# Kernel optimization log

Hardware: AMD Instinct MI355X
Metric: run time of the kernel (lower is better)

## Reference

```python
import jax, jax.numpy as jnp
import numpy as np

B, S, INPUT_DIM = 8, 512, 64
D_MODEL, NUM_LAYERS, OUTPUT_DIM = 512, 4, 10
D_INNER, D_STATE, D_CONV, DT_RANK = 2 * D_MODEL, 16, 4, 32
GRID_SIZE, SPLINE_K = 5, 3
N_COEFF = GRID_SIZE + SPLINE_K  # 8
_H = 2.0 / GRID_SIZE
GRID = jnp.linspace(-1.0 - SPLINE_K * _H, 1.0 + SPLINE_K * _H, GRID_SIZE + 2 * SPLINE_K + 1)


def b_splines(x):
    # x: (..., in) -> (..., in, N_COEFF) via Cox-de Boor recursion on fixed GRID
    x = x[..., None]
    b = ((x >= GRID[:-1]) & (x < GRID[1:])).astype(x.dtype)
    for p in range(1, SPLINE_K + 1):
        left = (x - GRID[:-(p + 1)]) / (GRID[p:-1] - GRID[:-(p + 1)])
        right = (GRID[p + 1:] - x) / (GRID[p + 1:] - GRID[1:-p])
        b = left * b[..., :-1] + right * b[..., 1:]
    return b


def kan(x, base_w, spline_w):
    # efficient-KAN: silu base path + per-edge spline path
    return jax.nn.silu(x) @ base_w.T + jnp.einsum('...ik,oik->...o', b_splines(x), spline_w)


def layernorm(x, g, b):
    m = jnp.mean(x, -1, keepdims=True)
    v = jnp.var(x, -1, keepdims=True)
    return (x - m) / jnp.sqrt(v + 1e-5) * g + b


def liquid_proj(x, Win, Wrec, b, tau):
    # liquid time-constant RNN: h' = (tanh(Wx + Uh + b) - h) / tau
    pre = x @ Win  # (B,S,H)
    tau_pos = jax.nn.softplus(tau) + 0.1
    def step(h, p):
        act = jnp.tanh(p + h @ Wrec + b)
        h = h + (act - h) / tau_pos
        return h, h
    h0 = jnp.zeros((x.shape[0], Win.shape[1]), x.dtype)
    hT, hs = jax.lax.scan(step, h0, pre.transpose(1, 0, 2))
    return hs.transpose(1, 0, 2), hT


def mamba_block(x, in_proj_w, conv_w, conv_b, x_proj_w, dt_proj_w, dt_proj_b, A_log, Dp, out_proj_w):
    Bb, Ss, _ = x.shape
    xz = x @ in_proj_w.T                       # (B,S,2*di)
    xm, z = jnp.split(xz, 2, axis=-1)
    # causal depthwise conv1d with kernel D_CONV
    xp = jnp.pad(xm, ((0, 0), (D_CONV - 1, 0), (0, 0)))
    xm = sum(xp[:, k:k + Ss, :] * conv_w[:, k] for k in range(D_CONV)) + conv_b
    xm = jax.nn.silu(xm)
    x_dbl = xm @ x_proj_w.T                    # (B,S,dt_rank+2n)
    dt, Bc, Cc = jnp.split(x_dbl, [DT_RANK, DT_RANK + D_STATE], axis=-1)
    dt = jax.nn.softplus(dt @ dt_proj_w.T + dt_proj_b)   # (B,S,di)
    A = -jnp.exp(A_log)                        # (di,n)
    dA = jnp.exp(dt[..., None] * A)            # (B,S,di,n)
    dBu = dt[..., None] * Bc[:, :, None, :] * xm[..., None]
    def step(h, inp):
        a, bu, c = inp
        h = a * h + bu
        return h, jnp.einsum('bdn,bn->bd', h, c)
    h0 = jnp.zeros((Bb, D_INNER, D_STATE), x.dtype)
    _, ys = jax.lax.scan(step, h0, (dA.transpose(1, 0, 2, 3), dBu.transpose(1, 0, 2, 3), Cc.transpose(1, 0, 2)))
    y = ys.transpose(1, 0, 2) + Dp * xm
    y = y * jax.nn.silu(z)
    return y @ out_proj_w.T


def forward(x, lq_Win, lq_Wrec, lq_b, lq_tau, ln_g, ln_b, in_proj_w, conv_w, conv_b,
            x_proj_w, dt_proj_w, dt_proj_b, A_log, Dp, out_proj_w,
            kan_base_w, kan_spline_w, fn_g, fn_b, cls_base_w, cls_spline_w):
    x, _ = liquid_proj(x, lq_Win, lq_Wrec, lq_b, lq_tau)
    for l in range(NUM_LAYERS):
        residual = x
        xn = layernorm(x, ln_g[l], ln_b[l])
        xm = mamba_block(xn, in_proj_w[l], conv_w[l], conv_b[l], x_proj_w[l],
                         dt_proj_w[l], dt_proj_b[l], A_log[l], Dp[l], out_proj_w[l])
        x = residual + kan(xm, kan_base_w[l], kan_spline_w[l])
    x = layernorm(x, fn_g, fn_b)
    return kan(x.mean(axis=1), cls_base_w, cls_spline_w)


def setup_inputs():
    key = jax.random.key(0)
    ks = jax.random.split(key, 12)
    n = lambda k, shape, s: jax.random.normal(k, shape, jnp.float32) * s
    return {
        "x": n(ks[0], (B, S, INPUT_DIM), 1.0),
        "lq_Win": n(ks[1], (INPUT_DIM, D_MODEL), INPUT_DIM ** -0.5),
        "lq_Wrec": n(ks[2], (D_MODEL, D_MODEL), D_MODEL ** -0.5),
        "lq_b": jnp.zeros((D_MODEL,), jnp.float32),
        "lq_tau": jnp.ones((D_MODEL,), jnp.float32),
        "ln_g": jnp.ones((NUM_LAYERS, D_MODEL), jnp.float32),
        "ln_b": jnp.zeros((NUM_LAYERS, D_MODEL), jnp.float32),
        "in_proj_w": n(ks[3], (NUM_LAYERS, 2 * D_INNER, D_MODEL), D_MODEL ** -0.5),
        "conv_w": n(ks[4], (NUM_LAYERS, D_INNER, D_CONV), D_CONV ** -0.5),
        "conv_b": jnp.zeros((NUM_LAYERS, D_INNER), jnp.float32),
        "x_proj_w": n(ks[5], (NUM_LAYERS, DT_RANK + 2 * D_STATE, D_INNER), D_INNER ** -0.5),
        "dt_proj_w": n(ks[6], (NUM_LAYERS, D_INNER, DT_RANK), DT_RANK ** -0.5),
        "dt_proj_b": jnp.full((NUM_LAYERS, D_INNER), float(np.log(np.expm1(0.01))), jnp.float32),
        "A_log": jnp.log(jnp.broadcast_to(jnp.arange(1, D_STATE + 1, dtype=jnp.float32), (NUM_LAYERS, D_INNER, D_STATE))),
        "Dp": jnp.ones((NUM_LAYERS, D_INNER), jnp.float32),
        "out_proj_w": n(ks[7], (NUM_LAYERS, D_MODEL, D_INNER), D_INNER ** -0.5),
        "kan_base_w": n(ks[8], (NUM_LAYERS, D_MODEL, D_MODEL), D_MODEL ** -0.5),
        "kan_spline_w": n(ks[9], (NUM_LAYERS, D_MODEL, D_MODEL, N_COEFF), 0.1 * D_MODEL ** -0.5),
        "fn_g": jnp.ones((D_MODEL,), jnp.float32),
        "fn_b": jnp.zeros((D_MODEL,), jnp.float32),
        "cls_base_w": n(ks[10], (OUTPUT_DIM, D_MODEL), D_MODEL ** -0.5),
        "cls_spline_w": n(ks[11], (OUTPUT_DIM, D_MODEL, N_COEFF), 0.1 * D_MODEL ** -0.5),
    }


def reference(x, lq_Win, lq_Wrec, lq_b, lq_tau, ln_g, ln_b, in_proj_w, conv_w, conv_b,
              x_proj_w, dt_proj_w, dt_proj_b, A_log, Dp, out_proj_w,
              kan_base_w, kan_spline_w, fn_g, fn_b, cls_base_w, cls_spline_w):
    return forward(x, lq_Win, lq_Wrec, lq_b, lq_tau, ln_g, ln_b, in_proj_w, conv_w, conv_b,
                   x_proj_w, dt_proj_w, dt_proj_b, A_log, Dp, out_proj_w,
                   kan_base_w, kan_spline_w, fn_g, fn_b, cls_base_w, cls_spline_w)
```

## Files before the change

kernel.cpp:

```cpp
#include <hip/hip_runtime.h>
#include <hip/hip_bf16.h>
#include <cmath>

#define DEV __device__ __forceinline__

constexpr int B_ = 8, S_ = 512, IN_ = 64, D_ = 512, L_ = 4;
constexpr int DI_ = 1024, DCONV_ = 4, DTR_ = 32;
constexpr int ROWS = B_ * S_;

constexpr size_t MB = 1ull << 20;
constexpr size_t OFF_X    = 0;
constexpr size_t OFF_XN   = OFF_X   + 8*MB;
constexpr size_t OFF_XZ   = OFF_XN  + 8*MB;
constexpr size_t OFF_XM   = OFF_XZ  + 32*MB;
constexpr size_t OFF_DT   = OFF_XM  + 16*MB;
constexpr size_t OFF_XDBL = OFF_DT  + 16*MB;
constexpr size_t OFF_YG   = OFF_XDBL+ 1*MB;
constexpr size_t OFF_MO   = OFF_YG  + 16*MB;
constexpr size_t OFF_WINT = OFF_MO  + 8*MB;
constexpr size_t OFF_MEAN = OFF_WINT+ 128*1024;
constexpr size_t OFF_HBUF = OFF_MEAN+ 16*1024;
constexpr size_t OFF_FLG  = OFF_HBUF+ 32*1024;
constexpr size_t OFF_W16  = OFF_FLG + 64*1024;
constexpr size_t OFF_BASIS= OFF_XZ;

constexpr size_t W_IP = 0;
constexpr size_t W_OP = 1048576;
constexpr size_t W_KB = 1572864;
constexpr size_t W_KS = 1835008;
constexpr size_t W_XP = 3932160;
constexpr size_t W_DT = 3997696;
constexpr size_t W_PER_LAYER = 4030464;

DEV float siluf(float x){ return x / (1.f + __expf(-x)); }
DEV float softplusf(float x){ return fmaxf(x, 0.f) + log1pf(__expf(-fabsf(x))); }
DEV unsigned short f2h(float f){ return __builtin_bit_cast(unsigned short, (_Float16)f); }
DEV int pk2(float a, float b){ return (int)((unsigned)f2h(a) | ((unsigned)f2h(b) << 16)); }

typedef _Float16 half8 __attribute__((ext_vector_type(8)));
typedef float f32x4 __attribute__((ext_vector_type(4)));

DEV void bspline8(float x, float* bb){
  const float h = 0.4f, g0 = -2.2f;
  float b0[11];
#pragma unroll
  for (int j = 0; j < 11; ++j){
    float gj  = g0 + h * j;
    float gj1 = g0 + h * (j + 1);
    b0[j] = (x >= gj && x < gj1) ? 1.f : 0.f;
  }
#pragma unroll
  for (int p = 1; p <= 3; ++p){
    float inv = 1.f / (h * p);
#pragma unroll
    for (int j = 0; j + p < 11; ++j){
      float gj  = g0 + h * j;
      float gip = g0 + h * (j + p + 1);
      b0[j] = (x - gj) * inv * b0[j] + (gip - x) * inv * b0[j + 1];
    }
  }
#pragma unroll
  for (int c = 0; c < 8; ++c) bb[c] = b0[c];
}

__global__ __launch_bounds__(256)
void conv_w16(const float* __restrict__ ip, const float* __restrict__ op,
              const float* __restrict__ kb, const float* __restrict__ ks,
              const float* __restrict__ xp, const float* __restrict__ dt,
              unsigned short* __restrict__ w16)
{
  int blk = blockIdx.x, tid = threadIdx.x;
  const float* src; size_t doff; int sb;
  if      (blk < 512) { src = ip; doff = W_IP; sb = blk; }
  else if (blk < 768) { src = op; doff = W_OP; sb = blk - 512; }
  else if (blk < 896) { src = kb; doff = W_KB; sb = blk - 768; }
  else if (blk < 1920){ src = ks; doff = W_KS; sb = blk - 896; }
  else if (blk < 1952){ src = xp; doff = W_XP; sb = blk - 1920; }
  else                { src = dt; doff = W_DT; sb = blk - 1952; }
  size_t e = (size_t)sb * 2048 + tid * 8;
  float4 a = *(const float4*)(src + e), b = *(const float4*)(src + e + 4);
  int4 v = { pk2(a.x,a.y), pk2(a.z,a.w), pk2(b.x,b.y), pk2(b.z,b.w) };
  *(int4*)&w16[doff + e] = v;
}

template<bool SILU_A, int EPI>
__global__ __launch_bounds__(256)
void gemm_nt(const float* __restrict__ A, int lda,
             const float* __restrict__ W, int ldw,
             float* __restrict__ C, int ldc,
             const float* __restrict__ bias, int K)
{
  __shared__ float As[16][68];
  __shared__ float Ws[16][68];
  const int tid = threadIdx.x;
  const int m0 = blockIdx.y * 64, n0 = blockIdx.x * 64;
  const int lr = tid >> 2, lc = (tid & 3) * 4;
  const float* Ap = A + (size_t)(m0 + lr) * lda + lc;
  const float* Wp = W + (size_t)(n0 + lr) * ldw + lc;
  const int tx = tid & 15, ty = tid >> 4;
  float acc[4][4] = {};
  for (int k0 = 0; k0 < K; k0 += 16){
    float4 a = *(const float4*)(Ap + k0);
    float4 w = *(const float4*)(Wp + k0);
    if (SILU_A){ a.x = siluf(a.x); a.y = siluf(a.y); a.z = siluf(a.z); a.w = siluf(a.w); }
    __syncthreads();
    As[lc+0][lr] = a.x; As[lc+1][lr] = a.y; As[lc+2][lr] = a.z; As[lc+3][lr] = a.w;
    Ws[lc+0][lr] = w.x; Ws[lc+1][lr] = w.y; Ws[lc+2][lr] = w.z; Ws[lc+3][lr] = w.w;
    __syncthreads();
#pragma unroll
    for (int k = 0; k < 16; ++k){
      float4 av = *(const float4*)&As[k][ty*4];
      float4 wv = *(const float4*)&Ws[k][tx*4];
      acc[0][0] += av.x*wv.x; acc[0][1] += av.x*wv.y; acc[0][2] += av.x*wv.z; acc[0][3] += av.x*wv.w;
      acc[1][0] += av.y*wv.x; acc[1][1] += av.y*wv.y; acc[1][2] += av.y*wv.z; acc[1][3] += av.y*wv.w;
      acc[2][0] += av.z*wv.x; acc[2][1] += av.z*wv.y; acc[2][2] += av.z*wv.z; acc[2][3] += av.z*wv.w;
      acc[3][0] += av.w*wv.x; acc[3][1] += av.w*wv.y; acc[3][2] += av.w*wv.z; acc[3][3] += av.w*wv.w;
    }
  }
#pragma unroll
  for (int i = 0; i < 4; ++i){
    float* Crow = C + (size_t)(m0 + ty*4 + i) * ldc + n0 + tx*4;
    float4 r = {acc[i][0], acc[i][1], acc[i][2], acc[i][3]};
    *(float4*)Crow = r;
  }
}


template<int AMODE, int EPI>
__global__ __launch_bounds__(256)
void gemm_h128(const void* __restrict__ Av, int lda,
               const unsigned short* __restrict__ W,
               float* __restrict__ C, int ldc,
               const float* __restrict__ bias, int K)
{
  __shared__ unsigned short As[128*40];
  __shared__ unsigned short Bs[128*40];
  const int tid = threadIdx.x;
  const int m0 = blockIdx.y * 128, n0 = blockIdx.x * 128;
  const int wid = tid >> 6, lane = tid & 63;
  const int wm = (wid & 1) * 64, wn = (wid >> 1) * 64;
  const int fr = lane & 15, fk = lane >> 4;
  const int sr = tid >> 1, sh = tid & 1;

  f32x4 acc[4][4];
#pragma unroll
  for (int i = 0; i < 4; ++i)
#pragma unroll
    for (int j = 0; j < 4; ++j)
#pragma unroll
      for (int r = 0; r < 4; ++r) acc[i][j][r] = 0.f;

  for (int k0 = 0; k0 < K; k0 += 32){
    int4 av0, av1;
    if (AMODE == 0){
      const unsigned short* ag = (const unsigned short*)Av + (size_t)(m0 + sr) * lda + k0 + sh*16;
      av0 = *(const int4*)ag; av1 = *(const int4*)(ag + 8);
    } else {
      const float* ag = (const float*)Av + (size_t)(m0 + sr) * lda + k0 + sh*16;
      float4 a0 = *(const float4*)ag,     a1 = *(const float4*)(ag+4);
      float4 a2 = *(const float4*)(ag+8), a3 = *(const float4*)(ag+12);
      if (AMODE == 2){
        a0.x=siluf(a0.x); a0.y=siluf(a0.y); a0.z=siluf(a0.z); a0.w=siluf(a0.w);
        a1.x=siluf(a1.x); a1.y=siluf(a1.y); a1.z=siluf(a1.z); a1.w=siluf(a1.w);
        a2.x=siluf(a2.x); a2.y=siluf(a2.y); a2.z=siluf(a2.z); a2.w=siluf(a2.w);
        a3.x=siluf(a3.x); a3.y=siluf(a3.y); a3.z=siluf(a3.z); a3.w=siluf(a3.w);
      }
      av0 = (int4){ pk2(a0.x,a0.y), pk2(a0.z,a0.w), pk2(a1.x,a1.y), pk2(a1.z,a1.w) };
      av1 = (int4){ pk2(a2.x,a2.y), pk2(a2.z,a2.w), pk2(a3.x,a3.y), pk2(a3.z,a3.w) };
    }
    const unsigned short* wg = W + (size_t)(n0 + sr) * K + k0 + sh*16;
    int4 bv0 = *(const int4*)wg, bv1 = *(const int4*)(wg + 8);
    __syncthreads();
    *(int4*)&As[sr*40 + sh*16]     = av0;
    *(int4*)&As[sr*40 + sh*16 + 8] = av1;
    *(int4*)&Bs[sr*40 + sh*16]     = bv0;
    *(int4*)&Bs[sr*40 + sh*16 + 8] = bv1;
    __syncthreads();
    half8 a[4], b[4];
#pragma unroll
    for (int i = 0; i < 4; ++i) a[i] = *(const half8*)&As[(wm + i*16 + fr)*40 + fk*8];
#pragma unroll
    for (int j = 0; j < 4; ++j) b[j] = *(const half8*)&Bs[(wn + j*16 + fr)*40 + fk*8];
#pragma unroll
    for (int i = 0; i < 4; ++i)
#pragma unroll
      for (int j = 0; j < 4; ++j)
        acc[i][j] = __builtin_amdgcn_mfma_f32_16x16x32_f16(a[i], b[j], acc[i][j], 0, 0, 0);
  }
#pragma unroll
  for (int i = 0; i < 4; ++i)
#pragma unroll
    for (int j = 0; j < 4; ++j){
      int col = n0 + wn + j*16 + fr;
#pragma unroll
      for (int r = 0; r < 4; ++r){
        int row = m0 + wm + i*16 + fk*4 + r;
        float* cp = C + (size_t)row * ldc + col;
        if (EPI == 0)      *cp = acc[i][j][r];
        else if (EPI == 1) *cp += acc[i][j][r];
        else               *cp = softplusf(acc[i][j][r] + bias[col]);
      }
    }
}

template<int AMODE, int EPI>
__global__ __launch_bounds__(256)
void gemm_h64(const void* __restrict__ Av, int lda,
              const unsigned short* __restrict__ W,
              float* __restrict__ C, int ldc,
              const float* __restrict__ bias, int K)
{
  __shared__ unsigned short As[128*40];
  __shared__ unsigned short Bs[64*40];
  const int tid = threadIdx.x;
  const int m0 = blockIdx.y * 128, n0 = blockIdx.x * 64;
  const int wid = tid >> 6, lane = tid & 63;
  const int fr = lane & 15, fk = lane >> 4;
  const int sr = tid >> 1, sh = tid & 1;
  const int br = tid >> 2, bq = tid & 3;

  f32x4 acc[2][4];
#pragma unroll
  for (int i = 0; i < 2; ++i)
#pragma unroll
    for (int j = 0; j < 4; ++j)
#pragma unroll
      for (int r = 0; r < 4; ++r) acc[i][j][r] = 0.f;

  for (int k0 = 0; k0 < K; k0 += 32){
    int4 av0, av1;
    if (AMODE == 0){
      const unsigned short* ag = (const unsigned short*)Av + (size_t)(m0 + sr) * lda + k0 + sh*16;
      av0 = *(const int4*)ag; av1 = *(const int4*)(ag + 8);
    } else {
      const float* ag = (const float*)Av + (size_t)(m0 + sr) * lda + k0 + sh*16;
      float4 a0 = *(const float4*)ag,     a1 = *(const float4*)(ag+4);
      float4 a2 = *(const float4*)(ag+8), a3 = *(const float4*)(ag+12);
      if (AMODE == 2){
        a0.x=siluf(a0.x); a0.y=siluf(a0.y); a0.z=siluf(a0.z); a0.w=siluf(a0.w);
        a1.x=siluf(a1.x); a1.y=siluf(a1.y); a1.z=siluf(a1.z); a1.w=siluf(a1.w);
        a2.x=siluf(a2.x); a2.y=siluf(a2.y); a2.z=siluf(a2.z); a2.w=siluf(a2.w);
        a3.x=siluf(a3.x); a3.y=siluf(a3.y); a3.z=siluf(a3.z); a3.w=siluf(a3.w);
      }
      av0 = (int4){ pk2(a0.x,a0.y), pk2(a0.z,a0.w), pk2(a1.x,a1.y), pk2(a1.z,a1.w) };
      av1 = (int4){ pk2(a2.x,a2.y), pk2(a2.z,a2.w), pk2(a3.x,a3.y), pk2(a3.z,a3.w) };
    }
    const unsigned short* wg = W + (size_t)(n0 + br) * K + k0 + bq*8;
    int4 bv0 = *(const int4*)wg;
    __syncthreads();
    *(int4*)&As[sr*40 + sh*16]     = av0;
    *(int4*)&As[sr*40 + sh*16 + 8] = av1;
    *(int4*)&Bs[br*40 + bq*8]      = bv0;
    __syncthreads();
    half8 a[2], b[4];
#pragma unroll
    for (int i = 0; i < 2; ++i) a[i] = *(const half8*)&As[(wid*32 + i*16 + fr)*40 + fk*8];
#pragma unroll
    for (int j = 0; j < 4; ++j) b[j] = *(const half8*)&Bs[(j*16 + fr)*40 + fk*8];
#pragma unroll
    for (int i = 0; i < 2; ++i)
#pragma unroll
      for (int j = 0; j < 4; ++j)
        acc[i][j] = __builtin_amdgcn_mfma_f32_16x16x32_f16(a[i], b[j], acc[i][j], 0, 0, 0);
  }
#pragma unroll
  for (int i = 0; i < 2; ++i)
#pragma unroll
    for (int j = 0; j < 4; ++j){
      int col = n0 + j*16 + fr;
#pragma unroll
      for (int r = 0; r < 4; ++r){
        int row = m0 + wid*32 + i*16 + fk*4 + r;
        float* cp = C + (size_t)row * ldc + col;
        if (EPI == 0)      *cp = acc[i][j][r];
        else if (EPI == 1) *cp += acc[i][j][r];
        else               *cp = softplusf(acc[i][j][r] + bias[col]);
      }
    }
}

__global__ __launch_bounds__(256)
void transpose_win(const float* __restrict__ Win, float* __restrict__ WinT)
{
  int idx = blockIdx.x * 256 + threadIdx.x;
  int n = idx >> 6, k = idx & 63;
  WinT[idx] = Win[(size_t)k * 512 + n];
}

__global__ __launch_bounds__(512)
void liquid_scan3(const float* __restrict__ pre, const float* __restrict__ Wrec,
                  const float* __restrict__ bias, const float* __restrict__ tau,
                  float* __restrict__ xout, float* __restrict__ hbuf,
                  unsigned* __restrict__ flags)
{
  __shared__ float Wl[32800];
  __shared__ float hl[544];
  __shared__ float hnew[64];
  const int tid = threadIdx.x;
  const int bid = blockIdx.x;
  const int slice = bid >> 3, b = bid & 7;
  for (int idx = tid; idx < 512*16; idx += 512){
    int k = idx >> 4, c4 = (idx & 15) * 4;
    float4 w = *(const float4*)(Wrec + (size_t)k*512 + slice*64 + c4);
    *(float4*)&Wl[k*64 + c4 + (k>>6)*4] = w;
  }
  hl[tid + (tid>>6)*4] = 0.f;
  const int o = tid >> 3, kl = tid & 7;
  const int og = slice*64 + o;
  const float tauinv = 1.f / (softplusf(tau[og]) + 0.1f);
  const float bo = bias[og];
  float hold = 0.f;
  const float* preb = pre + (size_t)b * S_ * 512;
  float* xb = xout + (size_t)b * S_ * 512;
  float* hb0 = hbuf + (size_t)b * 512;
  unsigned* bflags = flags + b*8*16;
  unsigned* myflag = bflags + slice*16;
  const int kbase = kl * 64;
  const float* wp = &Wl[(size_t)kbase*64 + o + kl*4];
  __syncthreads();
  for (int t = 0; t < S_; ++t){
    float prev = (kl == 0) ? preb[(size_t)t*512 + og] : 0.f;
    float hreg[64];
#pragma unroll
    for (int j4 = 0; j4 < 16; ++j4)
      *(float4*)&hreg[j4*4] = *(const float4*)&hl[kbase + kl*4 + j4*4];
    float s = 0.f;
#pragma unroll
    for (int j = 0; j < 64; ++j)
      s += hreg[j] * wp[(size_t)j * 64];
    s += __shfl_xor(s, 1);
    s += __shfl_xor(s, 2);
    s += __shfl_xor(s, 4);
    if (kl == 0){
      float act = tanhf(s + prev + bo);
      hold += (act - hold) * tauinv;
      xb[(size_t)t*512 + og] = hold;
      hnew[o] = hold;
    }
    __syncthreads();
    if (tid < 64)
      __hip_atomic_store(hb0 + (t&1)*4096 + slice*64 + tid, hnew[tid],
                         __ATOMIC_RELAXED, __HIP_MEMORY_SCOPE_AGENT);
    if (tid == 0){
      asm volatile("s_waitcnt vmcnt(0)" ::: "memory");
      __hip_atomic_store(myflag, (unsigned)(t+1),
                         __ATOMIC_RELAXED, __HIP_MEMORY_SCOPE_AGENT);
    }
    if (tid < 8){
      while (__hip_atomic_load(bflags + tid*16, __ATOMIC_RELAXED,
                               __HIP_MEMORY_SCOPE_AGENT) < (unsigned)(t+1))
        __builtin_amdgcn_s_sleep(1);
    }
    __syncthreads();
    float hv = __hip_atomic_load(hb0 + (t&1)*4096 + tid,
                                 __ATOMIC_RELAXED, __HIP_MEMORY_SCOPE_AGENT);
    hl[tid + (tid>>6)*4] = hv;
    __syncthreads();
  }
}

__global__ __launch_bounds__(256)
void conv_silu(const float* __restrict__ xz, const float* __restrict__ cw,
               const float* __restrict__ cb, float* __restrict__ xm)
{
  int idx = blockIdx.x * 256 + threadIdx.x;
  int d = idx & 1023;
  int bs = idx >> 10;
  int t = bs & 511;
  const float* p = xz + (size_t)bs * 2048 + d;
  float4 w = *(const float4*)(cw + d*4);
  float acc = cb[d] + w.w * p[0];
  if (t >= 1) acc += w.z * p[-2048];
  if (t >= 2) acc += w.y * p[-2*2048];
  if (t >= 3) acc += w.x * p[-3*2048];
  xm[idx] = siluf(acc);
}

__global__ __launch_bounds__(256)
void mamba_scan2(const float* __restrict__ dt, const float* __restrict__ xm,
                 const float* __restrict__ xdbl, const float* __restrict__ xz,
                 const float* __restrict__ A_log, const float* __restrict__ Dp,
                 unsigned short* __restrict__ yg)
{
  const int tid = threadIdx.x;
  const int wave = tid >> 6, lane = tid & 63;
  const int ch = lane >> 3, sub = lane & 7;
  const int d = blockIdx.x * 32 + wave * 8 + ch;
  const int b = blockIdx.y;
  float2 al = *(const float2*)(A_log + (size_t)d*16 + sub*2);
  const float A0 = -__expf(al.x), A1 = -__expf(al.y);
  const float Dv = Dp[d];
  float h0 = 0.f, h1 = 0.f;
  const size_t rb = (size_t)b * S_;
  const float* dtp = dt + rb*1024 + d;
  const float* xmp = xm + rb*1024 + d;
  const float* zp  = xz + rb*2048 + 1024 + d;
  const float* bcp = xdbl + rb*64 + 32 + sub*2;
  const float* ccp = xdbl + rb*64 + 48 + sub*2;
  unsigned short* yp = yg + rb*1024 + d;
#pragma unroll 2
  for (int t = 0; t < S_; ++t){
    float dtv = dtp[(size_t)t*1024];
    float xv  = xmp[(size_t)t*1024];
    float2 B2 = *(const float2*)(bcp + (size_t)t*64);
    float2 C2 = *(const float2*)(ccp + (size_t)t*64);
    float cbu = dtv * xv;
    h0 = __expf(dtv * A0) * h0 + cbu * B2.x;
    h1 = __expf(dtv * A1) * h1 + cbu * B2.y;
    float y = h0 * C2.x + h1 * C2.y;
    y += __shfl_xor(y, 1);
    y += __shfl_xor(y, 2);
    y += __shfl_xor(y, 4);
    if (sub == 0){
      float zv = zp[(size_t)t*2048];
      yp[(size_t)t*1024] = f2h((y + Dv * xv) * siluf(zv));
    }
  }
}

template<bool H>
__global__ __launch_bounds__(256)
void layernorm_k(const float* __restrict__ x, const float* __restrict__ g,
                 const float* __restrict__ b, void* __restrict__ y)
{
  __shared__ float red[8];
  const int row = blockIdx.x, tid = threadIdx.x;
  const float* xr = x + (size_t)row * 512;
  float2 v = *(const float2*)(xr + tid*2);
  float s = v.x + v.y;
#pragma unroll
  for (int o = 32; o; o >>= 1) s += __shfl_xor(s, o);
  if ((tid & 63) == 0) red[tid >> 6] = s;
  __syncthreads();
  float mean = (red[0] + red[1] + red[2] + red[3]) * (1.f/512.f);
  float dx = v.x - mean, dy = v.y - mean;
  float q = dx*dx + dy*dy;
#pragma unroll
  for (int o = 32; o; o >>= 1) q += __shfl_xor(q, o);
  if ((tid & 63) == 0) red[4 + (tid >> 6)] = q;
  __syncthreads();
  float var = (red[4] + red[5] + red[6] + red[7]) * (1.f/512.f);
  float rstd = rsqrtf(var + 1e-5f);
  float2 gg = *(const float2*)(g + tid*2);
  float2 bb = *(const float2*)(b + tid*2);
  float ox = dx*rstd*gg.x + bb.x;
  float oy = dy*rstd*gg.y + bb.y;
  if (H){
    unsigned* yr = (unsigned*)y + (size_t)row*256 + tid;
    *yr = (unsigned)f2h(ox) | ((unsigned)f2h(oy) << 16);
  } else {
    float2 o2 = {ox, oy};
    *(float2*)((float*)y + (size_t)row*512 + tid*2) = o2;
  }
}

__global__ __launch_bounds__(256)
void bspline_kernel(const float* __restrict__ xin, unsigned short* __restrict__ basis)
{
  int idx = blockIdx.x * 256 + threadIdx.x;
  float x = xin[idx];
  float bb[8];
  bspline8(x, bb);
  int4 v = { pk2(bb[0],bb[1]), pk2(bb[2],bb[3]), pk2(bb[4],bb[5]), pk2(bb[6],bb[7]) };
  *(int4*)(basis + (size_t)idx * 8) = v;
}

__global__ __launch_bounds__(512)
void mean_over_s(const float* __restrict__ x, float* __restrict__ out)
{
  int b = blockIdx.x, d = threadIdx.x;
  const float* p = x + (size_t)b*S_*512 + d;
  float s = 0.f;
  for (int t = 0; t < S_; ++t) s += p[(size_t)t*512];
  out[b*512 + d] = s * (1.f/512.f);
}

__global__ __launch_bounds__(64)
void cls_kan(const float* __restrict__ xmean, const float* __restrict__ bw,
             const float* __restrict__ sw, float* __restrict__ out)
{
  int o = blockIdx.x % 10, b = blockIdx.x / 10;
  int lane = threadIdx.x;
  float acc = 0.f;
  for (int i = lane; i < 512; i += 64){
    float xv = xmean[b*512 + i];
    acc += siluf(xv) * bw[o*512 + i];
    float bb[8]; bspline8(xv, bb);
    const float* sp = sw + ((size_t)(o*512 + i)) * 8;
#pragma unroll
    for (int c = 0; c < 8; ++c) acc += bb[c] * sp[c];
  }
#pragma unroll
  for (int off = 32; off; off >>= 1) acc += __shfl_xor(acc, off);
  if (lane == 0) out[b*10 + o] = acc;
}

extern "C" void kernel_launch(void* const* d_in, const int* in_sizes, int n_in,
                              void* d_out, int out_size, void* d_ws, size_t ws_size,
                              hipStream_t stream)
{
  const float* x_in    = (const float*)d_in[0];
  const float* lq_Win  = (const float*)d_in[1];
  const float* lq_Wrec = (const float*)d_in[2];
  const float* lq_b    = (const float*)d_in[3];
  const float* lq_tau  = (const float*)d_in[4];
  const float* ln_g    = (const float*)d_in[5];
  const float* ln_bi   = (const float*)d_in[6];
  const float* in_proj = (const float*)d_in[7];
  const float* conv_w  = (const float*)d_in[8];
  const float* conv_b  = (const float*)d_in[9];
  const float* x_proj  = (const float*)d_in[10];
  const float* dt_w    = (const float*)d_in[11];
  const float* dt_b    = (const float*)d_in[12];
  const float* A_log   = (const float*)d_in[13];
  const float* Dp      = (const float*)d_in[14];
  const float* out_w   = (const float*)d_in[15];
  const float* kb_w    = (const float*)d_in[16];
  const float* ks_w    = (const float*)d_in[17];
  const float* fn_g    = (const float*)d_in[18];
  const float* fn_b    = (const float*)d_in[19];
  const float* cb_w    = (const float*)d_in[20];
  const float* cs_w    = (const float*)d_in[21];
  float* out = (float*)d_out;

  char* ws = (char*)d_ws;
  float* xcur  = (float*)(ws + OFF_X);
  float* xn32  = (float*)(ws + OFF_XN);
  unsigned short* xn16 = (unsigned short*)(ws + OFF_XN);
  float* xz    = (float*)(ws + OFF_XZ);
  float* xm    = (float*)(ws + OFF_XM);
  float* dtb   = (float*)(ws + OFF_DT);
  float* xdbl  = (float*)(ws + OFF_XDBL);
  unsigned short* yg16 = (unsigned short*)(ws + OFF_YG);
  float* mo    = (float*)(ws + OFF_MO);
  float* wint  = (float*)(ws + OFF_WINT);
  float* xmean = (float*)(ws + OFF_MEAN);
  float* hbufp = (float*)(ws + OFF_HBUF);
  unsigned* flgp = (unsigned*)(ws + OFF_FLG);
  unsigned short* w16 = (unsigned short*)(ws + OFF_W16);
  unsigned short* basis = (unsigned short*)(ws + OFF_BASIS);

  transpose_win<<<128, 256, 0, stream>>>(lq_Win, wint);
  gemm_nt<false,0><<<dim3(D_/64, ROWS/64), 256, 0, stream>>>(x_in, IN_, wint, IN_, xn32, D_, nullptr, IN_);
  hipMemsetAsync(flgp, 0, 8*8*16*sizeof(unsigned), stream);
  liquid_scan3<<<64, 512, 0, stream>>>(xn32, lq_Wrec, lq_b, lq_tau, xcur, hbufp, flgp);

  for (int l = 0; l < L_; ++l){
    conv_w16<<<1968, 256, 0, stream>>>(
        in_proj + (size_t)l*2*DI_*D_, out_w + (size_t)l*D_*DI_,
        kb_w + (size_t)l*D_*D_, ks_w + (size_t)l*D_*D_*8,
        x_proj + (size_t)l*64*DI_, dt_w + (size_t)l*DI_*DTR_,
        w16 + (size_t)l*W_PER_LAYER);
  }

  for (int l = 0; l < L_; ++l){
    const unsigned short* wl = w16 + (size_t)l*W_PER_LAYER;
    layernorm_k<true><<<ROWS, 256, 0, stream>>>(xcur, ln_g + l*D_, ln_bi + l*D_, xn16);
    gemm_h128<0,0><<<dim3(16, 32), 256, 0, stream>>>(
        xn16, D_, wl + W_IP, xz, 2*DI_, nullptr, D_);
    conv_silu<<<ROWS*DI_/256, 256, 0, stream>>>(xz, conv_w + l*DI_*DCONV_, conv_b + l*DI_, xm);
    gemm_h64<1,0><<<dim3(1, 32), 256, 0, stream>>>(
        xm, DI_, wl + W_XP, xdbl, 64, nullptr, DI_);
    gemm_h128<1,2><<<dim3(8, 32), 256, 0, stream>>>(
        xdbl, 64, wl + W_DT, dtb, DI_, dt_b + l*DI_, DTR_);
    mamba_scan2<<<dim3(32, 8), 256, 0, stream>>>(
        dtb, xm, xdbl, xz, A_log + (size_t)l*DI_*16, Dp + l*DI_, yg16);
    gemm_h64<0,0><<<dim3(8, 32), 256, 0, stream>>>(
        yg16, DI_, wl + W_OP, mo, D_, nullptr, DI_);
    bspline_kernel<<<ROWS*D_/256, 256, 0, stream>>>(mo, basis);
    gemm_h64<2,1><<<dim3(8, 32), 256, 0, stream>>>(
        mo, D_, wl + W_KB, xcur, D_, nullptr, D_);
    gemm_h64<0,1><<<dim3(8, 32), 256, 0, stream>>>(
        basis, D_*8, wl + W_KS, xcur, D_, nullptr, D_*8);
  }

  layernorm_k<false><<<ROWS, 256, 0, stream>>>(xcur, fn_g, fn_b, xn32);
  mean_over_s<<<B_, 512, 0, stream>>>(xn32, xmean);
  cls_kan<<<B_*10, 64, 0, stream>>>(xmean, cb_w, cs_w, out);
}
```

Measured before the change: 3.853 ms.

## Fuse dt projection into Mamba scan, store xz/xm in fp16, split-K x_proj

```diff
diff --git a/kernel.cpp b/kernel.cpp
--- a/kernel.cpp
+++ b/kernel.cpp
@@ -35,6 +35,7 @@
 DEV float siluf(float x){ return x / (1.f + __expf(-x)); }
 DEV float softplusf(float x){ return fmaxf(x, 0.f) + log1pf(__expf(-fabsf(x))); }
 DEV unsigned short f2h(float f){ return __builtin_bit_cast(unsigned short, (_Float16)f); }
+DEV float h2f(unsigned short u){ return (float)__builtin_bit_cast(_Float16, u); }
 DEV int pk2(float a, float b){ return (int)((unsigned)f2h(a) | ((unsigned)f2h(b) << 16)); }
 
 typedef _Float16 half8 __attribute__((ext_vector_type(8)));
@@ -66,8 +67,7 @@
 __global__ __launch_bounds__(256)
 void conv_w16(const float* __restrict__ ip, const float* __restrict__ op,
               const float* __restrict__ kb, const float* __restrict__ ks,
-              const float* __restrict__ xp, const float* __restrict__ dt,
-              unsigned short* __restrict__ w16)
+              const float* __restrict__ xp, unsigned short* __restrict__ w16)
 {
   int blk = blockIdx.x, tid = threadIdx.x;
   const float* src; size_t doff; int sb;
@@ -75,8 +75,7 @@
   else if (blk < 768) { src = op; doff = W_OP; sb = blk - 512; }
   else if (blk < 896) { src = kb; doff = W_KB; sb = blk - 768; }
   else if (blk < 1920){ src = ks; doff = W_KS; sb = blk - 896; }
-  else if (blk < 1952){ src = xp; doff = W_XP; sb = blk - 1920; }
-  else                { src = dt; doff = W_DT; sb = blk - 1952; }
+  else                { src = xp; doff = W_XP; sb = blk - 1920; }
   size_t e = (size_t)sb * 2048 + tid * 8;
   float4 a = *(const float4*)(src + e), b = *(const float4*)(src + e + 4);
   int4 v = { pk2(a.x,a.y), pk2(a.z,a.w), pk2(b.x,b.y), pk2(b.z,b.w) };
@@ -126,12 +125,41 @@
 }
 
 
+template<int AMODE>
+DEV void stage_a(const void* Av, int lda, int m0, int sr, int k0, int sh,
+                 int4& av0, int4& av1)
+{
+  if (AMODE == 0){
+    const unsigned short* ag = (const unsigned short*)Av + (size_t)(m0 + sr) * lda + k0 + sh*16;
+    av0 = *(const int4*)ag; av1 = *(const int4*)(ag + 8);
+  } else {
+    const float* ag = (const float*)Av + (size_t)(m0 + sr) * lda + k0 + sh*16;
+    float4 a0 = *(const float4*)ag,     a1 = *(const float4*)(ag+4);
+    float4 a2 = *(const float4*)(ag+8), a3 = *(const float4*)(ag+12);
+    if (AMODE == 2){
+      a0.x=siluf(a0.x); a0.y=siluf(a0.y); a0.z=siluf(a0.z); a0.w=siluf(a0.w);
+      a1.x=siluf(a1.x); a1.y=siluf(a1.y); a1.z=siluf(a1.z); a1.w=siluf(a1.w);
+      a2.x=siluf(a2.x); a2.y=siluf(a2.y); a2.z=siluf(a2.z); a2.w=siluf(a2.w);
+      a3.x=siluf(a3.x); a3.y=siluf(a3.y); a3.z=siluf(a3.z); a3.w=siluf(a3.w);
+    }
+    av0 = (int4){ pk2(a0.x,a0.y), pk2(a0.z,a0.w), pk2(a1.x,a1.y), pk2(a1.z,a1.w) };
+    av1 = (int4){ pk2(a2.x,a2.y), pk2(a2.z,a2.w), pk2(a3.x,a3.y), pk2(a3.z,a3.w) };
+  }
+}
+
+DEV void epi_store(int EPI, void* Cv, size_t off, float v)
+{
+  if (EPI == 0)      ((float*)Cv)[off] = v;
+  else if (EPI == 1) ((float*)Cv)[off] += v;
+  else if (EPI == 3) ((unsigned short*)Cv)[off] = f2h(v);
+  else               atomicAdd((float*)Cv + off, v);
+}
+
 template<int AMODE, int EPI>
 __global__ __launch_bounds__(256)
 void gemm_h128(const void* __restrict__ Av, int lda,
                const unsigned short* __restrict__ W,
-               float* __restrict__ C, int ldc,
-               const float* __restrict__ bias, int K)
+               void* __restrict__ Cv, int ldc, int K)
 {
   __shared__ unsigned short As[128*40];
   __shared__ unsigned short Bs[128*40];
@@ -152,22 +180,7 @@
 
   for (int k0 = 0; k0 < K; k0 += 32){
     int4 av0, av1;
-    if (AMODE == 0){
-      const unsigned short* ag = (const unsigned short*)Av + (size_t)(m0 + sr) * lda + k0 + sh*16;
-      av0 = *(const int4*)ag; av1 = *(const int4*)(ag + 8);
-    } else {
-      const float* ag = (const float*)Av + (size_t)(m0 + sr) * lda + k0 + sh*16;
-      float4 a0 = *(const float4*)ag,     a1 = *(const float4*)(ag+4);
-      float4 a2 = *(const float4*)(ag+8), a3 = *(const float4*)(ag+12);
-      if (AMODE == 2){
-        a0.x=siluf(a0.x); a0.y=siluf(a0.y); a0.z=siluf(a0.z); a0.w=siluf(a0.w);
-        a1.x=siluf(a1.x); a1.y=siluf(a1.y); a1.z=siluf(a1.z); a1.w=siluf(a1.w);
-        a2.x=siluf(a2.x); a2.y=siluf(a2.y); a2.z=siluf(a2.z); a2.w=siluf(a2.w);
-        a3.x=siluf(a3.x); a3.y=siluf(a3.y); a3.z=siluf(a3.z); a3.w=siluf(a3.w);
-      }
-      av0 = (int4){ pk2(a0.x,a0.y), pk2(a0.z,a0.w), pk2(a1.x,a1.y), pk2(a1.z,a1.w) };
-      av1 = (int4){ pk2(a2.x,a2.y), pk2(a2.z,a2.w), pk2(a3.x,a3.y), pk2(a3.z,a3.w) };
-    }
+    stage_a<AMODE>(Av, lda, m0, sr, k0, sh, av0, av1);
     const unsigned short* wg = W + (size_t)(n0 + sr) * K + k0 + sh*16;
     int4 bv0 = *(const int4*)wg, bv1 = *(const int4*)(wg + 8);
     __syncthreads();
@@ -195,25 +208,22 @@
 #pragma unroll
       for (int r = 0; r < 4; ++r){
         int row = m0 + wm + i*16 + fk*4 + r;
-        float* cp = C + (size_t)row * ldc + col;
-        if (EPI == 0)      *cp = acc[i][j][r];
-        else if (EPI == 1) *cp += acc[i][j][r];
-        else               *cp = softplusf(acc[i][j][r] + bias[col]);
+        epi_store(EPI, Cv, (size_t)row * ldc + col, acc[i][j][r]);
       }
     }
 }
 
-template<int AMODE, int EPI>
+template<int AMODE, int EPI, int KSPLIT = 1>
 __global__ __launch_bounds__(256)
 void gemm_h64(const void* __restrict__ Av, int lda,
               const unsigned short* __restrict__ W,
-              float* __restrict__ C, int ldc,
-              const float* __restrict__ bias, int K)
+              void* __restrict__ Cv, int ldc, int K)
 {
   __shared__ unsigned short As[128*40];
   __shared__ unsigned short Bs[64*40];
   const int tid = threadIdx.x;
   const int m0 = blockIdx.y * 128, n0 = blockIdx.x * 64;
+  const int klen = K / KSPLIT, kbase = blockIdx.z * klen;
   const int wid = tid >> 6, lane = tid & 63;
   const int fr = lane & 15, fk = lane >> 4;
   const int sr = tid >> 1, sh = tid & 1;
@@ -227,24 +237,10 @@
 #pragma unroll
       for (int r = 0; r < 4; ++r) acc[i][j][r] = 0.f;
 
-  for (int k0 = 0; k0 < K; k0 += 32){
+  for (int kk = 0; kk < klen; kk += 32){
+    int k0 = kbase + kk;
     int4 av0, av1;
-    if (AMODE == 0){
-      const unsigned short* ag = (const unsigned short*)Av + (size_t)(m0 + sr) * lda + k0 + sh*16;
-      av0 = *(const int4*)ag; av1 = *(const int4*)(ag + 8);
-    } else {
-      const float* ag = (const float*)Av + (size_t)(m0 + sr) * lda + k0 + sh*16;
-      float4 a0 = *(const float4*)ag,     a1 = *(const float4*)(ag+4);
-      float4 a2 = *(const float4*)(ag+8), a3 = *(const float4*)(ag+12);
-      if (AMODE == 2){
-        a0.x=siluf(a0.x); a0.y=siluf(a0.y); a0.z=siluf(a0.z); a0.w=siluf(a0.w);
-        a1.x=siluf(a1.x); a1.y=siluf(a1.y); a1.z=siluf(a1.z); a1.w=siluf(a1.w);
-        a2.x=siluf(a2.x); a2.y=siluf(a2.y); a2.z=siluf(a2.z); a2.w=siluf(a2.w);
-        a3.x=siluf(a3.x); a3.y=siluf(a3.y); a3.z=siluf(a3.z); a3.w=siluf(a3.w);
-      }
-      av0 = (int4){ pk2(a0.x,a0.y), pk2(a0.z,a0.w), pk2(a1.x,a1.y), pk2(a1.z,a1.w) };
-      av1 = (int4){ pk2(a2.x,a2.y), pk2(a2.z,a2.w), pk2(a3.x,a3.y), pk2(a3.z,a3.w) };
-    }
+    stage_a<AMODE>(Av, lda, m0, sr, k0, sh, av0, av1);
     const unsigned short* wg = W + (size_t)(n0 + br) * K + k0 + bq*8;
     int4 bv0 = *(const int4*)wg;
     __syncthreads();
@@ -271,10 +267,7 @@
 #pragma unroll
       for (int r = 0; r < 4; ++r){
         int row = m0 + wid*32 + i*16 + fk*4 + r;
-        float* cp = C + (size_t)row * ldc + col;
-        if (EPI == 0)      *cp = acc[i][j][r];
-        else if (EPI == 1) *cp += acc[i][j][r];
-        else               *cp = softplusf(acc[i][j][r] + bias[col]);
+        epi_store(EPI, Cv, (size_t)row * ldc + col, acc[i][j][r]);
       }
     }
 }
@@ -348,8 +341,7 @@
     }
     if (tid < 8){
       while (__hip_atomic_load(bflags + tid*16, __ATOMIC_RELAXED,
-                               __HIP_MEMORY_SCOPE_AGENT) < (unsigned)(t+1))
-        __builtin_amdgcn_s_sleep(1);
+                               __HIP_MEMORY_SCOPE_AGENT) < (unsigned)(t+1)) { }
     }
     __syncthreads();
     float hv = __hip_atomic_load(hb0 + (t&1)*4096 + tid,
@@ -360,25 +352,26 @@
 }
 
 __global__ __launch_bounds__(256)
-void conv_silu(const float* __restrict__ xz, const float* __restrict__ cw,
-               const float* __restrict__ cb, float* __restrict__ xm)
+void conv_silu(const unsigned short* __restrict__ xz, const float* __restrict__ cw,
+               const float* __restrict__ cb, unsigned short* __restrict__ xm)
 {
   int idx = blockIdx.x * 256 + threadIdx.x;
   int d = idx & 1023;
   int bs = idx >> 10;
   int t = bs & 511;
-  const float* p = xz + (size_t)bs * 2048 + d;
+  const unsigned short* p = xz + (size_t)bs * 2048 + d;
   float4 w = *(const float4*)(cw + d*4);
-  float acc = cb[d] + w.w * p[0];
-  if (t >= 1) acc += w.z * p[-2048];
-  if (t >= 2) acc += w.y * p[-2*2048];
-  if (t >= 3) acc += w.x * p[-3*2048];
-  xm[idx] = siluf(acc);
-}
-
-__global__ __launch_bounds__(256)
-void mamba_scan2(const float* __restrict__ dt, const float* __restrict__ xm,
-                 const float* __restrict__ xdbl, const float* __restrict__ xz,
+  float acc = cb[d] + w.w * h2f(p[0]);
+  if (t >= 1) acc += w.z * h2f(p[-2048]);
+  if (t >= 2) acc += w.y * h2f(p[-2*2048]);
+  if (t >= 3) acc += w.x * h2f(p[-3*2048]);
+  xm[idx] = f2h(siluf(acc));
+}
+
+__global__ __launch_bounds__(256)
+void mamba_scan3(const float* __restrict__ xdbl, const unsigned short* __restrict__ xm,
+                 const unsigned short* __restrict__ xz,
+                 const float* __restrict__ dt_w, const float* __restrict__ dt_b,
                  const float* __restrict__ A_log, const float* __restrict__ Dp,
                  unsigned short* __restrict__ yg)
 {
@@ -390,20 +383,27 @@
   float2 al = *(const float2*)(A_log + (size_t)d*16 + sub*2);
   const float A0 = -__expf(al.x), A1 = -__expf(al.y);
   const float Dv = Dp[d];
+  const float4 wq = *(const float4*)(dt_w + (size_t)d*32 + sub*4);
+  const float dtbv = dt_b[d];
   float h0 = 0.f, h1 = 0.f;
   const size_t rb = (size_t)b * S_;
-  const float* dtp = dt + rb*1024 + d;
-  const float* xmp = xm + rb*1024 + d;
-  const float* zp  = xz + rb*2048 + 1024 + d;
-  const float* bcp = xdbl + rb*64 + 32 + sub*2;
-  const float* ccp = xdbl + rb*64 + 48 + sub*2;
+  const float* xdp = xdbl + rb*64;
+  const unsigned short* xmp = xm + rb*1024 + d;
+  const unsigned short* zp  = xz + rb*2048 + 1024 + d;
+  float* dummy;
   unsigned short* yp = yg + rb*1024 + d;
 #pragma unroll 2
   for (int t = 0; t < S_; ++t){
-    float dtv = dtp[(size_t)t*1024];
-    float xv  = xmp[(size_t)t*1024];
-    float2 B2 = *(const float2*)(bcp + (size_t)t*64);
-    float2 C2 = *(const float2*)(ccp + (size_t)t*64);
+    const float* xr = xdp + (size_t)t*64;
+    float4 xq = *(const float4*)(xr + sub*4);
+    float s = xq.x*wq.x + xq.y*wq.y + xq.z*wq.z + xq.w*wq.w;
+    s += __shfl_xor(s, 1);
+    s += __shfl_xor(s, 2);
+    s += __shfl_xor(s, 4);
+    float dtv = softplusf(s + dtbv);
+    float xv  = h2f(xmp[(size_t)t*1024]);
+    float2 B2 = *(const float2*)(xr + 32 + sub*2);
+    float2 C2 = *(const float2*)(xr + 48 + sub*2);
     float cbu = dtv * xv;
     h0 = __expf(dtv * A0) * h0 + cbu * B2.x;
     h1 = __expf(dtv * A1) * h1 + cbu * B2.y;
@@ -412,7 +412,7 @@
     y += __shfl_xor(y, 2);
     y += __shfl_xor(y, 4);
     if (sub == 0){
-      float zv = zp[(size_t)t*2048];
+      float zv = h2f(zp[(size_t)t*2048]);
       yp[(size_t)t*1024] = f2h((y + Dv * xv) * siluf(zv));
     }
   }
@@ -527,9 +527,8 @@
   float* xcur  = (float*)(ws + OFF_X);
   float* xn32  = (float*)(ws + OFF_XN);
   unsigned short* xn16 = (unsigned short*)(ws + OFF_XN);
-  float* xz    = (float*)(ws + OFF_XZ);
-  float* xm    = (float*)(ws + OFF_XM);
-  float* dtb   = (float*)(ws + OFF_DT);
+  unsigned short* xz16 = (unsigned short*)(ws + OFF_XZ);
+  unsigned short* xm16 = (unsigned short*)(ws + OFF_XM);
   float* xdbl  = (float*)(ws + OFF_XDBL);
   unsigned short* yg16 = (unsigned short*)(ws + OFF_YG);
   float* mo    = (float*)(ws + OFF_MO);
@@ -546,32 +545,31 @@
   liquid_scan3<<<64, 512, 0, stream>>>(xn32, lq_Wrec, lq_b, lq_tau, xcur, hbufp, flgp);
 
   for (int l = 0; l < L_; ++l){
-    conv_w16<<<1968, 256, 0, stream>>>(
+    conv_w16<<<1952, 256, 0, stream>>>(
         in_proj + (size_t)l*2*DI_*D_, out_w + (size_t)l*D_*DI_,
         kb_w + (size_t)l*D_*D_, ks_w + (size_t)l*D_*D_*8,
-        x_proj + (size_t)l*64*DI_, dt_w + (size_t)l*DI_*DTR_,
-        w16 + (size_t)l*W_PER_LAYER);
+        x_proj + (size_t)l*64*DI_, w16 + (size_t)l*W_PER_LAYER);
   }
 
   for (int l = 0; l < L_; ++l){
     const unsigned short* wl = w16 + (size_t)l*W_PER_LAYER;
     layernorm_k<true><<<ROWS, 256, 0, stream>>>(xcur, ln_g + l*D_, ln_bi + l*D_, xn16);
-    gemm_h128<0,0><<<dim3(16, 32), 256, 0, stream>>>(
-        xn16, D_, wl + W_IP, xz, 2*DI_, nullptr, D_);
-    conv_silu<<<ROWS*DI_/256, 256, 0, stream>>>(xz, conv_w + l*DI_*DCONV_, conv_b + l*DI_, xm);
-    gemm_h64<1,0><<<dim3(1, 32), 256, 0, stream>>>(
-        xm, DI_, wl + W_XP, xdbl, 64, nullptr, DI_);
-    gemm_h128<1,2><<<dim3(8, 32), 256, 0, stream>>>(
-        xdbl, 64, wl + W_DT, dtb, DI_, dt_b + l*DI_, DTR_);
-    mamba_scan2<<<dim3(32, 8), 256, 0, stream>>>(
-        dtb, xm, xdbl, xz, A_log + (size_t)l*DI_*16, Dp + l*DI_, yg16);
+    gemm_h128<0,3><<<dim3(16, 32), 256, 0, stream>>>(
+        xn16, D_, wl + W_IP, xz16, 2*DI_, D_);
+    conv_silu<<<ROWS*DI_/256, 256, 0, stream>>>(xz16, conv_w + l*DI_*DCONV_, conv_b + l*DI_, xm16);
+    hipMemsetAsync(xdbl, 0, (size_t)ROWS*64*sizeof(float), stream);
+    gemm_h64<0,5,4><<<dim3(1, 32, 4), 256, 0, stream>>>(
+        xm16, DI_, wl + W_XP, xdbl, 64, DI_);
+    mamba_scan3<<<dim3(32, 8), 256, 0, stream>>>(
+        xdbl, xm16, xz16, dt_w + (size_t)l*DI_*DTR_, dt_b + l*DI_,
+        A_log + (size_t)l*DI_*16, Dp + l*DI_, yg16);
     gemm_h64<0,0><<<dim3(8, 32), 256, 0, stream>>>(
-        yg16, DI_, wl + W_OP, mo, D_, nullptr, DI_);
+        yg16, DI_, wl + W_OP, mo, D_, DI_);
     bspline_kernel<<<ROWS*D_/256, 256, 0, stream>>>(mo, basis);
     gemm_h64<2,1><<<dim3(8, 32), 256, 0, stream>>>(
-        mo, D_, wl + W_KB, xcur, D_, nullptr, D_);
+        mo, D_, wl + W_KB, xcur, D_, D_);
     gemm_h64<0,1><<<dim3(8, 32), 256, 0, stream>>>(
-        basis, D_*8, wl + W_KS, xcur, D_, nullptr, D_*8);
+        basis, D_*8, wl + W_KS, xcur, D_, D_*8);
   }
 
   layernorm_k<false><<<ROWS, 256, 0, stream>>>(xcur, fn_g, fn_b, xn32);
```

Result: slower. 4.243 ms (+10.1%).
